# Performance work log

Hardware: AMD Instinct MI355X
Metric: run time of the kernel (lower is better)

The kernel has to match this reference:

```python
import jax, jax.numpy as jnp
import numpy as np

B, P, D_ENC, D_DEC, D_ATT, E, V, T = 64, 144, 1792, 512, 512, 300, 32000, 30
LN_EPS = 1e-5


def _ln(x, g, b):
    m = x.mean(-1, keepdims=True)
    v = jnp.var(x, axis=-1, keepdims=True)
    return (x - m) * jax.lax.rsqrt(v + LN_EPS) * g + b


def setup_inputs() -> dict:
    key = jax.random.key(0)
    ks = iter(jax.random.split(key, 40))
    r = lambda shape, s=0.02: (jax.random.normal(next(ks), shape, jnp.float32) * s)
    inp = {}
    inp['features'] = jax.random.normal(next(ks), (B, P, D_ENC), jnp.float32)
    inp['captions'] = jax.random.randint(next(ks), (B, T), 0, V, jnp.int32)
    inp['emb_table'] = r((V, E), 0.05)
    # attention params
    inp['ln_q_g'] = jnp.ones((D_DEC,), jnp.float32)
    inp['ln_q_b'] = jnp.zeros((D_DEC,), jnp.float32)
    inp['ln_kv_g'] = jnp.ones((D_ENC,), jnp.float32)
    inp['ln_kv_b'] = jnp.zeros((D_ENC,), jnp.float32)
    inp['Wq'] = r((D_DEC, D_ATT)); inp['bq'] = jnp.zeros((D_ATT,), jnp.float32)
    inp['Wk'] = r((D_ENC, D_ATT)); inp['bk'] = jnp.zeros((D_ATT,), jnp.float32)
    inp['Wbeta'] = r((D_DEC, 1)); inp['bbeta'] = jnp.zeros((1,), jnp.float32)
    # LSTM gate params, packed as [in_dim, 4*H] in gate order (i, f, o, g).
    # Context fed to the LSTM is the attention output of dim encoder_dim (V = normalized features).
    inp['Wh'] = r((D_DEC, 4 * D_DEC))
    inp['Wu'] = r((E, 4 * D_DEC))
    inp['Wa'] = r((D_ENC, 4 * D_DEC))
    inp['b_gates'] = jnp.zeros((4 * D_DEC,), jnp.float32)  # linear biases + extra b_* params combined
    # output head
    inp['W_Lh'] = r((D_DEC, E)); inp['b_Lh'] = jnp.zeros((E,), jnp.float32)
    inp['W_Lz'] = r((D_ENC, E)); inp['b_Lz'] = jnp.zeros((E,), jnp.float32)
    inp['W_Lo'] = r((E, V)); inp['b_Lo'] = jnp.zeros((V,), jnp.float32)
    # init state
    inp['W_ih'] = r((D_ENC, D_DEC)); inp['b_ih'] = jnp.zeros((D_DEC,), jnp.float32)
    inp['W_ic'] = r((D_ENC, D_DEC)); inp['b_ic'] = jnp.zeros((D_DEC,), jnp.float32)
    return inp


def reference(features, captions, emb_table, ln_q_g, ln_q_b, ln_kv_g, ln_kv_b,
              Wq, bq, Wk, bk, Wbeta, bbeta, Wh, Wu, Wa, b_gates,
              W_Lh, b_Lh, W_Lz, b_Lz, W_Lo, b_Lo, W_ih, b_ih, W_ic, b_ic):
    scale = jnp.sqrt(jnp.asarray(Wq.shape[1], jnp.float32))
    # features are constant across timesteps -> hoist ln_kv and K projection
    feats_n = _ln(features, ln_kv_g, ln_kv_b)          # [B,P,Denc]
    K = feats_n @ Wk + bk                               # [B,P,A]
    mean_a = features.mean(axis=1)                      # [B,Denc]
    h0 = mean_a @ W_ih + b_ih
    c0 = mean_a @ W_ic + b_ic
    embs = emb_table[captions]                          # [B,T,E] (dropout = identity in eval)
    xs = jnp.swapaxes(embs[:, :-1], 0, 1)               # [T-1,B,E], embedding at step t is word t-1

    def step(carry, emb_t):
        h, c = carry
        hq = _ln(h, ln_q_g, ln_q_b)                     # [B,H]
        Q = hq @ Wq + bq                                # [B,A]
        scores = jnp.einsum('ba,bpa->bp', Q, K) / scale
        alpha = jax.nn.softmax(scores, axis=-1)         # [B,P]
        context = jnp.einsum('bp,bpd->bd', alpha, feats_n)  # [B,Denc]
        beta = jax.nn.sigmoid(hq @ Wbeta + bbeta)       # [B,1]
        z = beta * context
        gates = h @ Wh + emb_t @ Wu + z @ Wa + b_gates  # [B,4H]
        i_t, f_t, o_t, g_t = jnp.split(gates, 4, axis=-1)
        c_new = jax.nn.sigmoid(f_t) * c + jax.nn.sigmoid(i_t) * jnp.tanh(g_t)
        h_new = jax.nn.sigmoid(o_t) * jnp.tanh(c_new)
        out_o = emb_t + (h_new @ W_Lh + b_Lh) + (z @ W_Lz + b_Lz)
        logits = out_o @ W_Lo + b_Lo                    # [B,V]
        return (h_new, c_new), (logits, alpha)

    _, (logits, alphas) = jax.lax.scan(step, (h0, c0), xs)
    # step t=0 stays zero, as in the original torch loop (range(1, seq_len))
    predictions = jnp.concatenate(
        [jnp.zeros((1,) + logits.shape[1:], logits.dtype), logits], axis=0).swapaxes(0, 1)
    alphas_out = jnp.concatenate(
        [jnp.zeros((1,) + alphas.shape[1:], alphas.dtype), alphas], axis=0).swapaxes(0, 1)
    return predictions, alphas_out
```

## Files before the change

### kernel.cpp

```cpp
#include <hip/hip_runtime.h>
#include <hip/hip_bf16.h>


#define NB 64
#define NP 144
#define DE 1792
#define DD 512
#define DA 512
#define EM 300
#define NV 32000
#define NTT 30
#define NS 29
#define G4 2048
#define KP 320
#define KG1 2304
#define LN_EPS 1e-5f
#define RSCALE 0.044194173824159216f
#define KSPL 12

typedef __attribute__((ext_vector_type(8))) short short8;
typedef __attribute__((ext_vector_type(4))) float f32x4;
typedef __attribute__((ext_vector_type(8))) unsigned short ushort8v;

__device__ __forceinline__ float bf2f(unsigned short u){
  union { unsigned int i; float f; } w; w.i = ((unsigned int)u) << 16; return w.f;
}
__device__ __forceinline__ unsigned short f2bf(float f){
  union { float f; unsigned int i; } u; u.f = f;
  unsigned int r = u.i + 0x7FFFu + ((u.i >> 16) & 1u);
  return (unsigned short)(r >> 16);
}
__device__ __forceinline__ float sigm(float x){ return 1.f/(1.f + __expf(-x)); }

__device__ __forceinline__ float wave_reduce_sum(float v){
  #pragma unroll
  for (int o = 32; o >= 1; o >>= 1) v += __shfl_xor(v, o);
  return v;
}
__device__ __forceinline__ float wave_reduce_max(float v){
  #pragma unroll
  for (int o = 32; o >= 1; o >>= 1) v = fmaxf(v, __shfl_xor(v, o));
  return v;
}
__device__ __forceinline__ float block_sum256(float v, float* sbuf){
  v = wave_reduce_sum(v);
  const int lane = threadIdx.x & 63, wid = threadIdx.x >> 6;
  if (lane == 0) sbuf[wid] = v;
  __syncthreads();
  const float r = sbuf[0] + sbuf[1] + sbuf[2] + sbuf[3];
  __syncthreads();
  return r;
}
__device__ __forceinline__ float block_sum512(float v, float* sbuf8){
  v = wave_reduce_sum(v);
  const int lane = threadIdx.x & 63, wid = threadIdx.x >> 6;
  if (lane == 0) sbuf8[wid] = v;
  __syncthreads();
  float r = 0.f;
  #pragma unroll
  for (int i = 0; i < 8; ++i) r += sbuf8[i];
  __syncthreads();
  return r;
}

__device__ __forceinline__ void stage_tile(const unsigned short* __restrict__ src,
    int row_stride, int k0, char* lds){
  const int tid = threadIdx.x;
  #pragma unroll
  for (int c = 0; c < 2; ++c){
    const int o = tid + c*256;
    const int m = o >> 3, ks8 = o & 7;
    const ushort8v v = *(const ushort8v*)&src[(size_t)m*row_stride + k0 + ks8*8];
    *(ushort8v*)&lds[m*128 + ((ks8 ^ (m&7))<<4)] = v;
  }
}
__device__ __forceinline__ void mma64(const char* Alds, const char* Blds,
    int w, int lane, f32x4 acc[4]){
  #pragma unroll
  for (int ks = 0; ks < 2; ++ks){
    const int slot = ks*4 + (lane>>4);
    const int n = w*16 + (lane&15);
    const short8 bfv = *(const short8*)&Blds[n*128 + ((slot ^ (n&7))<<4)];
    #pragma unroll
    for (int fm = 0; fm < 4; ++fm){
      const int m = fm*16 + (lane&15);
      const short8 afv = *(const short8*)&Alds[m*128 + ((slot ^ (m&7))<<4)];
      acc[fm] = __builtin_amdgcn_mfma_f32_16x16x32_bf16(afv, bfv, acc[fm], 0, 0, 0);
    }
  }
}

__global__ __launch_bounds__(256) void k_zero(float* __restrict__ pred,
                                              float* __restrict__ alph){
  const int idx = blockIdx.x * 256 + threadIdx.x;
  {
    const int b = idx / NV, v = idx - b * NV;
    pred[(size_t)b * NTT * NV + v] = 0.f;
  }
  if (idx < NB * NP){
    const int b = idx / NP, p = idx - b * NP;
    alph[(size_t)b * NTT * NP + p] = 0.f;
  }
}

__global__ __launch_bounds__(256) void k_ln_feats(const float* __restrict__ feats,
    const float* __restrict__ g, const float* __restrict__ bb,
    unsigned short* __restrict__ out){
  __shared__ float sbuf[4];
  const int row = blockIdx.x;
  const float* x = feats + (size_t)row * DE;
  float v[7]; float s = 0.f;
  #pragma unroll
  for (int i = 0; i < 7; ++i){ v[i] = x[i*256 + threadIdx.x]; s += v[i]; }
  const float mean = block_sum256(s, sbuf) * (1.f/DE);
  float q = 0.f;
  #pragma unroll
  for (int i = 0; i < 7; ++i){ const float d = v[i] - mean; q += d*d; }
  const float var = block_sum256(q, sbuf) * (1.f/DE);
  const float rinv = rsqrtf(var + LN_EPS);
  #pragma unroll
  for (int i = 0; i < 7; ++i){
    const int idx = i*256 + threadIdx.x;
    out[(size_t)row*DE + idx] = f2bf((v[i]-mean)*rinv*g[idx] + bb[idx]);
  }
}

__global__ __launch_bounds__(256) void k_mean(const float* __restrict__ feats,
                                              float* __restrict__ mean_a){
  const int idx = blockIdx.x * 256 + threadIdx.x;
  const int b = idx / DE, d = idx - b * DE;
  const float* p = feats + (size_t)b * NP * DE + d;
  float s = 0.f;
  for (int pp = 0; pp < NP; ++pp) s += p[(size_t)pp * DE];
  mean_a[idx] = s * (1.f/NP);
}

__global__ __launch_bounds__(256) void k_cvt_T(const float* __restrict__ src,
    unsigned short* __restrict__ dst, const int K, const int N, const int KPad){
  __shared__ float t[64][65];
  const int n0 = blockIdx.x*64, k0 = blockIdx.y*64;
  for (int i = threadIdx.x; i < 4096; i += 256){
    const int k = i>>6, n = i&63;
    t[k][n] = (k0 + k < K) ? src[(size_t)(k0+k)*N + n0+n] : 0.f;
  }
  __syncthreads();
  for (int i = threadIdx.x; i < 4096; i += 256){
    const int n = i>>6, k = i&63;
    dst[(size_t)(n0+n)*KPad + k0+k] = f2bf(t[k][n]);
  }
}

__global__ __launch_bounds__(256) void k_cvt_wlt(const float* __restrict__ W_Lh,
    const float* __restrict__ W_Lz, unsigned short* __restrict__ WLt){
  __shared__ float t[64][65];
  const int e0 = blockIdx.x*64, k0 = blockIdx.y*64;
  for (int i = threadIdx.x; i < 4096; i += 256){
    const int k = i>>6, e2 = i&63;
    const int kg = k0 + k, e = e0 + e2;
    float v = 0.f;
    if (e < EM) v = (kg < DD) ? W_Lh[(size_t)kg*EM + e] : W_Lz[(size_t)(kg-DD)*EM + e];
    t[k][e2] = v;
  }
  __syncthreads();
  for (int i = threadIdx.x; i < 4096; i += 256){
    const int e2 = i>>6, k = i&63;
    WLt[(size_t)(e0+e2)*KG1 + k0+k] = f2bf(t[k][e2]);
  }
}

__global__ __launch_bounds__(256) void k_wg(const float* __restrict__ Wq,
    const float* __restrict__ g, unsigned short* __restrict__ Wg){
  const int idx = blockIdx.x*256 + threadIdx.x;
  const int k = idx >> 9;
  Wg[idx] = f2bf(g[k]*Wq[idx]);
}

__global__ __launch_bounds__(512) void k_pre_vq(const float* __restrict__ Wq,
    const float* __restrict__ bk, float* __restrict__ vq){
  const int k = threadIdx.x;
  const float* row = Wq + (size_t)k*DA;
  float acc = 0.f;
  for (int a = 0; a < DA; ++a) acc = fmaf(row[a], bk[a], acc);
  vq[k] = acc;
}

__global__ __launch_bounds__(512) void k_uvoff(const float* __restrict__ Wq,
    const float* __restrict__ g, const float* __restrict__ bln,
    const float* __restrict__ bq, const float* __restrict__ Wbeta,
    const float* __restrict__ bbeta, const float* __restrict__ bk,
    float* __restrict__ u_, float* __restrict__ voff,
    float* __restrict__ gw, float* __restrict__ cscal){
  __shared__ float sbuf8[8];
  const int a = threadIdx.x;
  float uu = 0.f, vv = 0.f;
  for (int k = 0; k < DD; ++k){
    const float wv = Wq[(size_t)k*DA + a];
    uu = fmaf(g[k],   wv, uu);
    vv = fmaf(bln[k], wv, vv);
  }
  const float vo = vv + bq[a];
  u_[a]   = uu;
  voff[a] = vo;
  gw[a]   = g[a]*Wbeta[a];
  const float c1 = block_sum512(g[a]*Wbeta[a], sbuf8);
  const float c2 = block_sum512(bln[a]*Wbeta[a], sbuf8);
  const float c3 = block_sum512(uu*bk[a], sbuf8);
  const float c4 = block_sum512(vo*bk[a], sbuf8);
  if (a == 0){ cscal[0]=c1; cscal[1]=c2+bbeta[0]; cscal[2]=c3; cscal[3]=c4; }
}

__global__ __launch_bounds__(256) void k_KF(const unsigned short* __restrict__ fb,
    const unsigned short* __restrict__ WkT, unsigned short* __restrict__ KF){
  __shared__ char Alds[8192];
  __shared__ char Blds[8192];
  const int mt = blockIdx.x, nt = blockIdx.y;
  const int tid = threadIdx.x, w = tid>>6, lane = tid&63;
  f32x4 acc[4];
  #pragma unroll
  for (int i = 0; i < 4; ++i) acc[i] = (f32x4)(0.f);
  for (int kt = 0; kt < 28; ++kt){
    __syncthreads();
    stage_tile(fb  + (size_t)mt*64*DE, DE, kt*64, Alds);
    stage_tile(WkT + (size_t)nt*64*DE, DE, kt*64, Blds);
    __syncthreads();
    mma64(Alds, Blds, w, lane, acc);
  }
  const int q = nt*64 + w*16 + (lane&15);
  #pragma unroll
  for (int fm = 0; fm < 4; ++fm)
    #pragma unroll
    for (int r = 0; r < 4; ++r){
      const int row = mt*64 + fm*16 + (lane>>4)*4 + r;
      KF[(size_t)row*DD + q] = f2bf(acc[fm][r]);
    }
}

__global__ __launch_bounds__(256) void k_QG2(const unsigned short* __restrict__ KF,
    const unsigned short* __restrict__ Wg, const float* __restrict__ g_,
    const float* __restrict__ vq, unsigned short* __restrict__ G2){
  __shared__ char Alds[8192];
  __shared__ char Blds[8192];
  const int mt = blockIdx.x, nt = blockIdx.y;
  const int tid = threadIdx.x, w = tid>>6, lane = tid&63;
  f32x4 acc[4];
  #pragma unroll
  for (int i = 0; i < 4; ++i) acc[i] = (f32x4)(0.f);
  for (int kt = 0; kt < 8; ++kt){
    __syncthreads();
    stage_tile(KF + (size_t)mt*64*DD, DD, kt*64, Alds);
    stage_tile(Wg + (size_t)nt*64*DD, DD, kt*64, Blds);
    __syncthreads();
    mma64(Alds, Blds, w, lane, acc);
  }
  const int q = nt*64 + w*16 + (lane&15);
  const float add = g_[q]*vq[q];
  #pragma unroll
  for (int fm = 0; fm < 4; ++fm)
    #pragma unroll
    for (int r = 0; r < 4; ++r){
      const int row = mt*64 + fm*16 + (lane>>4)*4 + r;
      G2[(size_t)row*DD + q] = f2bf(acc[fm][r] + add);
    }
}

__global__ __launch_bounds__(512) void k_sc12(const unsigned short* __restrict__ KF,
    const float* __restrict__ u_, const float* __restrict__ voff,
    const float* __restrict__ cscal, float2* __restrict__ sc12){
  const int w = threadIdx.x>>6, lane = threadIdx.x&63;
  const int row = blockIdx.x*8 + w;
  const unsigned short* kf = KF + (size_t)row*DD + lane*8;
  float s1 = 0.f, s2 = 0.f;
  #pragma unroll
  for (int j = 0; j < 8; ++j){
    const float kv = bf2f(kf[j]);
    s1 = fmaf(u_[lane*8 + j],   kv, s1);
    s2 = fmaf(voff[lane*8 + j], kv, s2);
  }
  s1 = wave_reduce_sum(s1);
  s2 = wave_reduce_sum(s2);
  if (lane == 0){
    float2 o; o.x = s1 + cscal[2]; o.y = s2 + cscal[3];
    sc12[row] = o;
  }
}

__global__ __launch_bounds__(256) void k_init_g(const float* __restrict__ mean_a,
    const float* __restrict__ W, const float* __restrict__ bias,
    float* __restrict__ out, unsigned short* __restrict__ outbf){
  __shared__ float la[64*68];
  __shared__ float lb[64*68];
  const int j0 = blockIdx.x*64;
  const int tid = threadIdx.x, tr = tid&15, tn = tid>>4;
  float acc[16] = {0.f};
  for (int a0 = 0; a0 < DE; a0 += 64){
    __syncthreads();
    for (int i = tid; i < 4096; i += 256){
      const int b = i>>6, k = i&63;
      la[k*68 + b] = mean_a[(size_t)b*DE + a0+k];
    }
    for (int i = tid; i < 4096; i += 256){
      const int k = i>>6, j = i&63;
      lb[k*68 + j] = W[(size_t)(a0+k)*DD + j0+j];
    }
    __syncthreads();
    for (int k = 0; k < 64; ++k){
      float av[4], bv[4];
      #pragma unroll
      for (int ii = 0; ii < 4; ++ii) av[ii] = la[k*68 + tr*4+ii];
      #pragma unroll
      for (int jj = 0; jj < 4; ++jj) bv[jj] = lb[k*68 + tn*4+jj];
      #pragma unroll
      for (int ii = 0; ii < 4; ++ii)
        #pragma unroll
        for (int jj = 0; jj < 4; ++jj)
          acc[ii*4+jj] = fmaf(av[ii], bv[jj], acc[ii*4+jj]);
    }
  }
  #pragma unroll
  for (int ii = 0; ii < 4; ++ii)
    #pragma unroll
    for (int jj = 0; jj < 4; ++jj){
      const size_t idx = (size_t)(tr*4+ii)*DD + j0 + tn*4+jj;
      const float val = acc[ii*4+jj] + bias[j0 + tn*4+jj];
      out[idx] = val;
      if (outbf) outbf[idx] = f2bf(val);
    }
}

__global__ __launch_bounds__(256) void k_EU(const float* __restrict__ emb_table,
    const int* __restrict__ captions, const unsigned short* __restrict__ wut,
    float* __restrict__ eu){
  __shared__ char Alds[8192];
  __shared__ char Blds[8192];
  __shared__ int capL[64];
  const int jt = blockIdx.x, s = blockIdx.y;
  const int tid = threadIdx.x, w = tid>>6, lane = tid&63;
  if (tid < 64) capL[tid] = captions[tid*NTT + s];
  f32x4 acc[4];
  #pragma unroll
  for (int i = 0; i < 4; ++i) acc[i] = (f32x4)(0.f);
  for (int kt = 0; kt < 5; ++kt){
    __syncthreads();
    #pragma unroll
    for (int c = 0; c < 2; ++c){
      const int o = tid + c*256;
      const int m = o>>3, ks8 = o&7;
      const int e0 = kt*64 + ks8*8;
      const float* er = emb_table + (size_t)capL[m]*EM;
      ushort8v v;
      #pragma unroll
      for (int jj = 0; jj < 8; ++jj)
        v[jj] = (e0 + jj < EM) ? f2bf(er[e0 + jj]) : (unsigned short)0;
      *(ushort8v*)&Alds[m*128 + ((ks8 ^ (m&7))<<4)] = v;
    }
    stage_tile(wut + (size_t)jt*64*KP, KP, kt*64, Blds);
    __syncthreads();
    mma64(Alds, Blds, w, lane, acc);
  }
  const int j = jt*64 + w*16 + (lane&15);
  #pragma unroll
  for (int fm = 0; fm < 4; ++fm)
    #pragma unroll
    for (int r = 0; r < 4; ++r){
      const int b = fm*16 + (lane>>4)*4 + r;
      eu[((size_t)s*NB + b)*G4 + j] = acc[fm][r];
    }
}

__global__ __launch_bounds__(512) void k_A(
    const unsigned short* __restrict__ gp, const float* __restrict__ eu,
    const float* __restrict__ b_gates, const float* __restrict__ cin,
    float* __restrict__ cout, unsigned short* __restrict__ hst,
    const unsigned short* __restrict__ G2, const float2* __restrict__ sc12,
    const unsigned short* __restrict__ fb, const float* __restrict__ gw,
    const float* __restrict__ cscal, const int s, const int do_att,
    float* __restrict__ alph, unsigned short* __restrict__ zbf){
  __shared__ alignas(16) unsigned short hL[DD];
  __shared__ float sc[NP];
  __shared__ float al[NP];
  __shared__ float sredA[8*4];
  __shared__ float sbufM[8];
  __shared__ float sbufS[8];
  int sl, b;
  if (gridDim.x == 1){ sl = 0; b = blockIdx.y; }
  else {
    const int lin = blockIdx.x + 2*blockIdx.y;
    const int xcd = lin & 7, i = lin >> 3;
    b = xcd*8 + (i & 7);
    sl = i >> 3;
  }
  const int tid = threadIdx.x;
  const int w = tid>>6, lane = tid&63;
  float hn;
  if (s == 0){
    const unsigned short hb = hst[(size_t)b*DD + tid];
    hn = bf2f(hb);
    hL[tid] = hb;
  } else {
    const int m = s - 1;
    unsigned short gv[4*KSPL];
    #pragma unroll
    for (int ks = 0; ks < KSPL; ++ks){
      const unsigned short* gr = gp + ((size_t)ks*NB + b)*G4 + tid;
      gv[ks*4+0] = gr[0];
      gv[ks*4+1] = gr[DD];
      gv[ks*4+2] = gr[2*DD];
      gv[ks*4+3] = gr[3*DD];
    }
    const float* eur = eu + ((size_t)m*NB + b)*G4 + tid;
    float gs0 = b_gates[tid]        + eur[0];
    float gs1 = b_gates[DD + tid]   + eur[DD];
    float gs2 = b_gates[2*DD + tid] + eur[2*DD];
    float gs3 = b_gates[3*DD + tid] + eur[3*DD];
    #pragma unroll
    for (int ks = 0; ks < KSPL; ++ks){
      gs0 += bf2f(gv[ks*4+0]); gs1 += bf2f(gv[ks*4+1]);
      gs2 += bf2f(gv[ks*4+2]); gs3 += bf2f(gv[ks*4+3]);
    }
    const size_t idx = (size_t)b*DD + tid;
    const float cn = sigm(gs1)*cin[idx] + sigm(gs0)*tanhf(gs3);
    hn = sigm(gs2)*tanhf(cn);
    cout[idx] = cn;
    const unsigned short hb = f2bf(hn);
    hst[(size_t)s*NB*DD + idx] = hb;
    hL[tid] = hb;
  }
  if (!do_att) return;
  float p1 = hn, p2 = hn*hn, p3 = hn*gw[tid];
  #pragma unroll
  for (int o = 32; o >= 1; o >>= 1){
    p1 += __shfl_xor(p1, o);
    p2 += __shfl_xor(p2, o);
    p3 += __shfl_xor(p3, o);
  }
  if (lane == 0){ sredA[w*4] = p1; sredA[w*4+1] = p2; sredA[w*4+2] = p3; }
  __syncthreads();
  float S1 = 0.f, S2 = 0.f, S3 = 0.f;
  #pragma unroll
  for (int i = 0; i < 8; ++i){
    S1 += sredA[i*4]; S2 += sredA[i*4+1]; S3 += sredA[i*4+2];
  }
  const float mean = S1*(1.f/512.f);
  const float var  = S2*(1.f/512.f) - mean*mean;
  const float rinv = rsqrtf(var + LN_EPS);
  const float beta = sigm(rinv*(S3 - mean*cscal[0]) + cscal[1]);
  const short8 hv = *(const short8*)&hL[lane*8];
  #pragma unroll 1
  for (int i0 = 0; i0 < 18; i0 += 6){
    short8 U[6];
    float2 SV[6];
    #pragma unroll
    for (int j = 0; j < 6; ++j){
      const int p = w + 8*(i0+j);
      U[j] = *(const short8*)&G2[(size_t)(b*NP + p)*DD + lane*8];
      if (lane == 0) SV[j] = sc12[b*NP + p];
    }
    #pragma unroll
    for (int j = 0; j < 6; ++j){
      float a2 = 0.f;
      #pragma unroll
      for (int q = 0; q < 8; ++q)
        a2 = fmaf(bf2f((unsigned short)U[j][q]), bf2f((unsigned short)hv[q]), a2);
      a2 = wave_reduce_sum(a2);
      if (lane == 0)
        sc[w + 8*(i0+j)] = RSCALE*(rinv*a2 - rinv*mean*SV[j].x + SV[j].y);
    }
  }
  __syncthreads();
  const float v = (tid < NP) ? sc[tid] : -1e30f;
  const float mv = wave_reduce_max(v);
  if (lane == 0) sbufM[w] = mv;
  __syncthreads();
  float mm = sbufM[0];
  #pragma unroll
  for (int i = 1; i < 8; ++i) mm = fmaxf(mm, sbufM[i]);
  const float e = (tid < NP) ? __expf(v - mm) : 0.f;
  const float sv = wave_reduce_sum(e);
  if (lane == 0) sbufS[w] = sv;
  __syncthreads();
  float ssum = 0.f;
  #pragma unroll
  for (int i = 0; i < 8; ++i) ssum += sbufS[i];
  if (tid < NP){
    const float a3 = e / ssum;
    al[tid] = a3;
    if (sl == 0) alph[((size_t)b*NTT + s + 1)*NP + tid] = a3;
  }
  __syncthreads();
  if (tid < 448){
    const int d0 = sl*896 + tid*2;
    const unsigned short* fB = fb + (size_t)b*NP*DE + d0;
    float a0 = 0.f, a1 = 0.f;
    #pragma unroll 1
    for (int p0 = 0; p0 < NP; p0 += 12){
      ushort2 fv[12];
      #pragma unroll
      for (int j = 0; j < 12; ++j) fv[j] = *(const ushort2*)&fB[(size_t)(p0+j)*DE];
      #pragma unroll
      for (int j = 0; j < 12; ++j){
        const float ap = al[p0+j];
        a0 = fmaf(ap, bf2f(fv[j].x), a0);
        a1 = fmaf(ap, bf2f(fv[j].y), a1);
      }
    }
    ushort2 zo;
    zo.x = f2bf(a0*beta);
    zo.y = f2bf(a1*beta);
    *(ushort2*)&zbf[((size_t)s*NB + b)*DE + d0] = zo;
  }
}

__global__ __launch_bounds__(256) void k_B(
    const unsigned short* __restrict__ hst, const unsigned short* __restrict__ zbf,
    const unsigned short* __restrict__ whT, const unsigned short* __restrict__ wat,
    const int s, unsigned short* __restrict__ gp){
  __shared__ char Alds[8192];
  __shared__ char Blds[8192];
  const int jt = blockIdx.x, ks = blockIdx.y;
  const int tid = threadIdx.x, w = tid>>6, lane = tid&63;
  const unsigned short* hrow = hst + (size_t)s*NB*DD;
  const unsigned short* zrow = zbf + (size_t)s*NB*DE;
  f32x4 acc[4];
  #pragma unroll
  for (int i = 0; i < 4; ++i) acc[i] = (f32x4)(0.f);
  for (int kt = 0; kt < 3; ++kt){
    const int k0 = ks*192 + kt*64;
    __syncthreads();
    if (k0 < DD) stage_tile(hrow, DD, k0, Alds);
    else         stage_tile(zrow, DE, k0 - DD, Alds);
    #pragma unroll
    for (int c2 = 0; c2 < 2; ++c2){
      const int o = tid + c2*256;
      const int m = o>>3, ks8 = o&7;
      const int col = (m>>4)*DD + jt*16 + (m&15);
      const unsigned short* src = (k0 < DD)
          ? whT + (size_t)col*DD + k0
          : wat + (size_t)col*DE + (k0 - DD);
      const ushort8v v = *(const ushort8v*)&src[ks8*8];
      *(ushort8v*)&Blds[m*128 + ((ks8 ^ (m&7))<<4)] = v;
    }
    __syncthreads();
    mma64(Alds, Blds, w, lane, acc);
  }
  const int jcol = jt*16 + (lane&15);
  unsigned short* gps = gp + (size_t)ks*NB*G4;
  #pragma unroll
  for (int fm = 0; fm < 4; ++fm)
    #pragma unroll
    for (int r = 0; r < 4; ++r){
      const int b = fm*16 + (lane>>4)*4 + r;
      gps[(size_t)b*G4 + w*DD + jcol] = f2bf(acc[fm][r]);
    }
}

__global__ __launch_bounds__(256) void k_G1m(const unsigned short* __restrict__ hstbf,
    const unsigned short* __restrict__ zbf, const unsigned short* __restrict__ WLt,
    float* __restrict__ g1p){
  __shared__ char Alds[8192];
  __shared__ char Blds[8192];
  const int e0 = blockIdx.x*64, s = blockIdx.y, ks6 = blockIdx.z;
  const int tid = threadIdx.x, w = tid>>6, lane = tid&63;
  const unsigned short* hrow = hstbf + (size_t)(s+1)*NB*DD;
  const unsigned short* zrow = zbf + (size_t)s*NB*DE;
  f32x4 acc[4];
  #pragma unroll
  for (int i = 0; i < 4; ++i) acc[i] = (f32x4)(0.f);
  for (int kt = 0; kt < 6; ++kt){
    const int k0 = ks6*384 + kt*64;
    __syncthreads();
    if (k0 < DD) stage_tile(hrow, DD, k0, Alds);
    else         stage_tile(zrow, DE, k0 - DD, Alds);
    stage_tile(WLt + (size_t)e0*KG1, KG1, k0, Blds);
    __syncthreads();
    mma64(Alds, Blds, w, lane, acc);
  }
  const int e = e0 + w*16 + (lane&15);
  float* dst = g1p + (size_t)ks6*NS*NB*KP;
  #pragma unroll
  for (int fm = 0; fm < 4; ++fm)
    #pragma unroll
    for (int r = 0; r < 4; ++r){
      const int b = fm*16 + (lane>>4)*4 + r;
      dst[((size_t)s*NB + b)*KP + e] = acc[fm][r];
    }
}

__global__ __launch_bounds__(256) void k_G1red(const float* __restrict__ g1p,
    const float* __restrict__ b_Lh, const float* __restrict__ b_Lz,
    const float* __restrict__ emb_table, const int* __restrict__ captions,
    unsigned short* __restrict__ outo){
  const int idx = blockIdx.x*256 + threadIdx.x;
  const int row = idx / KP, e = idx - row*KP;
  const int s = row >> 6, b = row & 63;
  float v = 0.f;
  #pragma unroll
  for (int ks6 = 0; ks6 < 6; ++ks6) v += g1p[(size_t)ks6*NS*NB*KP + idx];
  if (e < EM){
    const int cap = captions[b*NTT + s];
    v += b_Lh[e] + b_Lz[e] + emb_table[(size_t)cap*EM + e];
  } else v = 0.f;
  outo[idx] = f2bf(v);
}

__global__ __launch_bounds__(256) void k_G2(const unsigned short* __restrict__ Abf,
    const unsigned short* __restrict__ Bt, const float* __restrict__ b_Lo,
    float* __restrict__ pred){
  __shared__ char Alds[128*128];
  __shared__ char Blds[256*128];
  const int bid = blockIdx.x;
  const int xcd = bid & 7, idx8 = bid >> 3;
  const int wgid = (xcd < 3 ? xcd*235 : 705 + (xcd-3)*234) + idx8;
  const int nt = wgid / 15, mt = wgid - nt*15;
  const int tid = threadIdx.x, w = tid>>6, lane = tid&63;
  f32x4 acc[8][4];
  #pragma unroll
  for (int i = 0; i < 8; ++i)
    #pragma unroll
    for (int j = 0; j < 4; ++j)
      acc[i][j] = (f32x4)(0.f);
  for (int kt = 0; kt < 5; ++kt){
    const int k0 = kt*64;
    __syncthreads();
    #pragma unroll
    for (int c2 = 0; c2 < 4; ++c2){
      const int o16 = tid + c2*256;
      const int m = o16>>3, ks8 = o16&7;
      const ushort8v v = *(const ushort8v*)&Abf[(size_t)(mt*128+m)*KP + k0 + ks8*8];
      *(ushort8v*)&Alds[m*128 + ((ks8 ^ (m&7))<<4)] = v;
    }
    #pragma unroll
    for (int c2 = 0; c2 < 8; ++c2){
      const int o16 = tid + c2*256;
      const int n = o16>>3, ks8 = o16&7;
      const ushort8v v = *(const ushort8v*)&Bt[(size_t)(nt*256+n)*KP + k0 + ks8*8];
      *(ushort8v*)&Blds[n*128 + ((ks8 ^ (n&7))<<4)] = v;
    }
    __syncthreads();
    #pragma unroll
    for (int ks = 0; ks < 2; ++ks){
      const int slot = ks*4 + (lane>>4);
      short8 af[8];
      #pragma unroll
      for (int fm = 0; fm < 8; ++fm){
        const int m = fm*16 + (lane&15);
        af[fm] = *(const short8*)&Alds[m*128 + ((slot ^ (m&7))<<4)];
      }
      #pragma unroll
      for (int fn = 0; fn < 4; ++fn){
        const int n = w*64 + fn*16 + (lane&15);
        const short8 bfv = *(const short8*)&Blds[n*128 + ((slot ^ (n&7))<<4)];
        #pragma unroll
        for (int fm = 0; fm < 8; ++fm)
          acc[fm][fn] = __builtin_amdgcn_mfma_f32_16x16x32_bf16(af[fm], bfv, acc[fm][fn], 0, 0, 0);
      }
    }
  }
  const int ncol0 = nt*256 + w*64 + (lane&15);
  #pragma unroll
  for (int fm = 0; fm < 8; ++fm){
    #pragma unroll
    for (int r = 0; r < 4; ++r){
      const int row = mt*128 + fm*16 + (lane>>4)*4 + r;
      if (row < NS*NB){
        const int s = row >> 6, b = row & 63;
        float* prow = &pred[((size_t)b*NTT + s + 1)*NV + ncol0];
        #pragma unroll
        for (int fn = 0; fn < 4; ++fn)
          __builtin_nontemporal_store(acc[fm][fn][r] + b_Lo[ncol0 + fn*16],
                                      &prow[fn*16]);
      }
    }
  }
}

extern "C" void kernel_launch(void* const* d_in, const int* in_sizes, int n_in,
                              void* d_out, int out_size, void* d_ws, size_t ws_size,
                              hipStream_t stream){
  const float* features  = (const float*)d_in[0];
  const int*   captions  = (const int*)  d_in[1];
  const float* emb_table = (const float*)d_in[2];
  const float* ln_q_g = (const float*)d_in[3];
  const float* ln_q_b = (const float*)d_in[4];
  const float* ln_kv_g= (const float*)d_in[5];
  const float* ln_kv_b= (const float*)d_in[6];
  const float* Wq     = (const float*)d_in[7];
  const float* bq     = (const float*)d_in[8];
  const float* Wk     = (const float*)d_in[9];
  const float* bk     = (const float*)d_in[10];
  const float* Wbeta  = (const float*)d_in[11];
  const float* bbeta  = (const float*)d_in[12];
  const float* Wh     = (const float*)d_in[13];
  const float* Wu     = (const float*)d_in[14];
  const float* Wa     = (const float*)d_in[15];
  const float* b_gates= (const float*)d_in[16];
  const float* W_Lh   = (const float*)d_in[17];
  const float* b_Lh   = (const float*)d_in[18];
  const float* W_Lz   = (const float*)d_in[19];
  const float* b_Lz   = (const float*)d_in[20];
  const float* W_Lo   = (const float*)d_in[21];
  const float* b_Lo   = (const float*)d_in[22];
  const float* W_ih   = (const float*)d_in[23];
  const float* b_ih   = (const float*)d_in[24];
  const float* W_ic   = (const float*)d_in[25];
  const float* b_ic   = (const float*)d_in[26];

  float* pred = (float*)d_out;
  float* alph = pred + (size_t)NB * NTT * NV;

  char* w = (char*)d_ws;
  auto alloc = [&](size_t bytes) -> void* {
    void* p = (void*)w; w += (bytes + 255) & ~(size_t)255; return p;
  };
  unsigned short* feats_bf = (unsigned short*)alloc((size_t)NB*NP*DE * 2);
  unsigned short* wlo_t    = (unsigned short*)alloc((size_t)NV*KP * 2);
  unsigned short* whT      = (unsigned short*)alloc((size_t)G4*DD * 2);
  unsigned short* wut      = (unsigned short*)alloc((size_t)G4*KP * 2);
  unsigned short* wat      = (unsigned short*)alloc((size_t)G4*DE * 2);
  unsigned short* WkT      = (unsigned short*)alloc((size_t)DD*DE * 2);
  unsigned short* WLt      = (unsigned short*)alloc((size_t)KP*KG1 * 2);
  unsigned short* Wg       = (unsigned short*)alloc((size_t)DD*DD * 2);
  unsigned short* KFbf     = (unsigned short*)alloc((size_t)NB*NP*DD * 2);
  unsigned short* G2bf     = (unsigned short*)alloc((size_t)NB*NP*DD * 2);
  float2* sc12  = (float2*)alloc((size_t)NB*NP * 8);
  float* vq     = (float*)alloc((size_t)DD * 4);
  float* u_     = (float*)alloc((size_t)DD * 4);
  float* voff   = (float*)alloc((size_t)DD * 4);
  float* gw     = (float*)alloc((size_t)DD * 4);
  float* cscal  = (float*)alloc(16);
  float* mean_a = (float*)alloc((size_t)NB*DE * 4);
  float* hbuf   = (float*)alloc((size_t)NB*DD * 4);
  float* cb0    = (float*)alloc((size_t)NB*DD * 4);
  float* cb1    = (float*)alloc((size_t)NB*DD * 4);
  unsigned short* hstbf = (unsigned short*)alloc((size_t)(NS+1)*NB*DD * 2);
  unsigned short* zbf   = (unsigned short*)alloc((size_t)NS*NB*DE * 2);
  unsigned short* outo  = (unsigned short*)alloc((size_t)1920*KP * 2);
  unsigned short* gp    = (unsigned short*)alloc((size_t)KSPL*NB*G4 * 2);
  float* eu_all = (float*)alloc((size_t)NS*NB*G4 * 4);
  float* g1p    = (float*)alloc((size_t)6*NS*NB*KP * 4);
  float* cb[2] = { cb0, cb1 };

  k_zero<<<dim3((NB*NV)/256), dim3(256), 0, stream>>>(pred, alph);
  k_ln_feats<<<dim3(NB*NP), dim3(256), 0, stream>>>(features, ln_kv_g, ln_kv_b, feats_bf);
  k_mean<<<dim3((NB*DE)/256), dim3(256), 0, stream>>>(features, mean_a);
  k_cvt_T<<<dim3(NV/64, KP/64), dim3(256), 0, stream>>>(W_Lo, wlo_t, EM, NV, KP);
  k_cvt_T<<<dim3(G4/64, DD/64), dim3(256), 0, stream>>>(Wh, whT, DD, G4, DD);
  k_cvt_T<<<dim3(G4/64, KP/64), dim3(256), 0, stream>>>(Wu, wut, EM, G4, KP);
  k_cvt_T<<<dim3(G4/64, DE/64), dim3(256), 0, stream>>>(Wa, wat, DE, G4, DE);
  k_cvt_T<<<dim3(DD/64, DE/64), dim3(256), 0, stream>>>(Wk, WkT, DE, DD, DE);
  k_cvt_wlt<<<dim3(KP/64, KG1/64), dim3(256), 0, stream>>>(W_Lh, W_Lz, WLt);
  k_wg<<<dim3((DD*DD)/256), dim3(256), 0, stream>>>(Wq, ln_q_g, Wg);
  k_pre_vq<<<dim3(1), dim3(512), 0, stream>>>(Wq, bk, vq);
  k_uvoff<<<dim3(1), dim3(512), 0, stream>>>(Wq, ln_q_g, ln_q_b, bq, Wbeta, bbeta,
      bk, u_, voff, gw, cscal);
  k_KF<<<dim3(NB*NP/64, DD/64), dim3(256), 0, stream>>>(feats_bf, WkT, KFbf);
  k_QG2<<<dim3(NB*NP/64, DD/64), dim3(256), 0, stream>>>(KFbf, Wg, ln_q_g, vq, G2bf);
  k_sc12<<<dim3(NB*NP/8), dim3(512), 0, stream>>>(KFbf, u_, voff, cscal, sc12);
  k_init_g<<<dim3(DD/64), dim3(256), 0, stream>>>(mean_a, W_ih, b_ih, hbuf, hstbf);
  k_init_g<<<dim3(DD/64), dim3(256), 0, stream>>>(mean_a, W_ic, b_ic, cb0, nullptr);
  k_EU<<<dim3(G4/64, NS), dim3(256), 0, stream>>>(emb_table, captions, wut, eu_all);

  for (int s = 0; s < NS; ++s){
    k_A<<<dim3(2, NB), dim3(512), 0, stream>>>(gp, eu_all, b_gates,
        cb[(s & 1) ^ 1], cb[s & 1], hstbf, G2bf, sc12, feats_bf,
        gw, cscal, s, 1, alph, zbf);
    k_B<<<dim3(32, KSPL), dim3(256), 0, stream>>>(hstbf, zbf, whT, wat, s, gp);
  }
  k_A<<<dim3(1, NB), dim3(512), 0, stream>>>(gp, eu_all, b_gates,
      cb[(NS & 1) ^ 1], cb[NS & 1], hstbf, G2bf, sc12, feats_bf,
      gw, cscal, NS, 0, alph, zbf);

  k_G1m<<<dim3(5, NS, 6), dim3(256), 0, stream>>>(hstbf, zbf, WLt, g1p);
  k_G1red<<<dim3((NS*NB*KP)/256), dim3(256), 0, stream>>>(g1p, b_Lh, b_Lz,
      emb_table, captions, outo);
  k_G2<<<dim3(1875), dim3(256), 0, stream>>>(outo, wlo_t, b_Lo, pred);
}
```

Before: 1.318 ms.

## Use 128x256 MFMA tiles with XCD-aware block mapping for K/G2 GEMMs

The K-projection and G2 GEMMs move from 64x64 tiles on a 144x8 grid to 128x256 tiles on 144 blocks, reusing the shared gemm_big routine (factored out of the logits GEMM). Block ids are remapped so consecutive blocks spread across the eight XCDs. The larger tiles cut redundant global loads and raise MFMA work per LDS stage, but leave only 144 blocks on the device. Separately, the per-step attention kernel batches more loads in flight (9 G2 rows and 36 feature rows per iteration), which raises register pressure.

```diff
diff --git a/kernel.cpp b/kernel.cpp
--- a/kernel.cpp
+++ b/kernel.cpp
@@ -90,6 +90,50 @@
   }
 }
 
+template <int NKT>
+__device__ __forceinline__ void gemm_big(const unsigned short* __restrict__ A,
+    const unsigned short* __restrict__ B, int sa, int sb,
+    char* Alds, char* Blds, int mt, int nt, f32x4 acc[8][4]){
+  const int tid = threadIdx.x, w = tid>>6, lane = tid&63;
+  for (int kt = 0; kt < NKT; ++kt){
+    const int k0 = kt*64;
+    __syncthreads();
+    #pragma unroll
+    for (int c2 = 0; c2 < 4; ++c2){
+      const int o16 = tid + c2*256;
+      const int m = o16>>3, ks8 = o16&7;
+      const ushort8v v = *(const ushort8v*)&A[(size_t)(mt*128+m)*sa + k0 + ks8*8];
+      *(ushort8v*)&Alds[m*128 + ((ks8 ^ (m&7))<<4)] = v;
+    }
+    #pragma unroll
+    for (int c2 = 0; c2 < 8; ++c2){
+      const int o16 = tid + c2*256;
+      const int n = o16>>3, ks8 = o16&7;
+      const ushort8v v = *(const ushort8v*)&B[(size_t)(nt*256+n)*sb + k0 + ks8*8];
+      *(ushort8v*)&Blds[n*128 + ((ks8 ^ (n&7))<<4)] = v;
+    }
+    __syncthreads();
+    #pragma unroll
+    for (int ks = 0; ks < 2; ++ks){
+      const int slot = ks*4 + (lane>>4);
+      short8 af[8];
+      #pragma unroll
+      for (int fm = 0; fm < 8; ++fm){
+        const int m = fm*16 + (lane&15);
+        af[fm] = *(const short8*)&Alds[m*128 + ((slot ^ (m&7))<<4)];
+      }
+      #pragma unroll
+      for (int fn = 0; fn < 4; ++fn){
+        const int n = w*64 + fn*16 + (lane&15);
+        const short8 bfv = *(const short8*)&Blds[n*128 + ((slot ^ (n&7))<<4)];
+        #pragma unroll
+        for (int fm = 0; fm < 8; ++fm)
+          acc[fm][fn] = __builtin_amdgcn_mfma_f32_16x16x32_bf16(af[fm], bfv, acc[fm][fn], 0, 0, 0);
+      }
+    }
+  }
+}
+
 __global__ __launch_bounds__(256) void k_zero(float* __restrict__ pred,
                                               float* __restrict__ alph){
   const int idx = blockIdx.x * 256 + threadIdx.x;
@@ -211,55 +255,60 @@
 
 __global__ __launch_bounds__(256) void k_KF(const unsigned short* __restrict__ fb,
     const unsigned short* __restrict__ WkT, unsigned short* __restrict__ KF){
-  __shared__ char Alds[8192];
-  __shared__ char Blds[8192];
-  const int mt = blockIdx.x, nt = blockIdx.y;
+  __shared__ char Alds[128*128];
+  __shared__ char Blds[256*128];
+  const int bid = blockIdx.x;
+  const int wgid = (bid & 7)*18 + (bid >> 3);
+  const int nt = wgid & 1, mt = wgid >> 1;
   const int tid = threadIdx.x, w = tid>>6, lane = tid&63;
-  f32x4 acc[4];
-  #pragma unroll
-  for (int i = 0; i < 4; ++i) acc[i] = (f32x4)(0.f);
-  for (int kt = 0; kt < 28; ++kt){
-    __syncthreads();
-    stage_tile(fb  + (size_t)mt*64*DE, DE, kt*64, Alds);
-    stage_tile(WkT + (size_t)nt*64*DE, DE, kt*64, Blds);
-    __syncthreads();
-    mma64(Alds, Blds, w, lane, acc);
-  }
-  const int q = nt*64 + w*16 + (lane&15);
-  #pragma unroll
-  for (int fm = 0; fm < 4; ++fm)
+  f32x4 acc[8][4];
+  #pragma unroll
+  for (int i = 0; i < 8; ++i)
+    #pragma unroll
+    for (int j = 0; j < 4; ++j) acc[i][j] = (f32x4)(0.f);
+  gemm_big<28>(fb, WkT, DE, DE, Alds, Blds, mt, nt, acc);
+  const int ncol0 = nt*256 + w*64 + (lane&15);
+  #pragma unroll
+  for (int fm = 0; fm < 8; ++fm)
     #pragma unroll
     for (int r = 0; r < 4; ++r){
-      const int row = mt*64 + fm*16 + (lane>>4)*4 + r;
-      KF[(size_t)row*DD + q] = f2bf(acc[fm][r]);
+      const int row = mt*128 + fm*16 + (lane>>4)*4 + r;
+      #pragma unroll
+      for (int fn = 0; fn < 4; ++fn)
+        KF[(size_t)row*DD + ncol0 + fn*16] = f2bf(acc[fm][fn][r]);
     }
 }
 
 __global__ __launch_bounds__(256) void k_QG2(const unsigned short* __restrict__ KF,
     const unsigned short* __restrict__ Wg, const float* __restrict__ g_,
     const float* __restrict__ vq, unsigned short* __restrict__ G2){
-  __shared__ char Alds[8192];
-  __shared__ char Blds[8192];
-  const int mt = blockIdx.x, nt = blockIdx.y;
+  __shared__ char Alds[128*128];
+  __shared__ char Blds[256*128];
+  const int bid = blockIdx.x;
+  const int wgid = (bid & 7)*18 + (bid >> 3);
+  const int nt = wgid & 1, mt = wgid >> 1;
   const int tid = threadIdx.x, w = tid>>6, lane = tid&63;
-  f32x4 acc[4];
-  #pragma unroll
-  for (int i = 0; i < 4; ++i) acc[i] = (f32x4)(0.f);
-  for (int kt = 0; kt < 8; ++kt){
-    __syncthreads();
-    stage_tile(KF + (size_t)mt*64*DD, DD, kt*64, Alds);
-    stage_tile(Wg + (size_t)nt*64*DD, DD, kt*64, Blds);
-    __syncthreads();
-    mma64(Alds, Blds, w, lane, acc);
-  }
-  const int q = nt*64 + w*16 + (lane&15);
-  const float add = g_[q]*vq[q];
-  #pragma unroll
-  for (int fm = 0; fm < 4; ++fm)
+  f32x4 acc[8][4];
+  #pragma unroll
+  for (int i = 0; i < 8; ++i)
+    #pragma unroll
+    for (int j = 0; j < 4; ++j) acc[i][j] = (f32x4)(0.f);
+  gemm_big<8>(KF, Wg, DD, DD, Alds, Blds, mt, nt, acc);
+  const int ncol0 = nt*256 + w*64 + (lane&15);
+  float addv[4];
+  #pragma unroll
+  for (int fn = 0; fn < 4; ++fn){
+    const int q = ncol0 + fn*16;
+    addv[fn] = g_[q]*vq[q];
+  }
+  #pragma unroll
+  for (int fm = 0; fm < 8; ++fm)
     #pragma unroll
     for (int r = 0; r < 4; ++r){
-      const int row = mt*64 + fm*16 + (lane>>4)*4 + r;
-      G2[(size_t)row*DD + q] = f2bf(acc[fm][r] + add);
+      const int row = mt*128 + fm*16 + (lane>>4)*4 + r;
+      #pragma unroll
+      for (int fn = 0; fn < 4; ++fn)
+        G2[(size_t)row*DD + ncol0 + fn*16] = f2bf(acc[fm][fn][r] + addv[fn]);
     }
 }
 
@@ -446,17 +495,17 @@
   const float beta = sigm(rinv*(S3 - mean*cscal[0]) + cscal[1]);
   const short8 hv = *(const short8*)&hL[lane*8];
   #pragma unroll 1
-  for (int i0 = 0; i0 < 18; i0 += 6){
-    short8 U[6];
-    float2 SV[6];
-    #pragma unroll
-    for (int j = 0; j < 6; ++j){
+  for (int i0 = 0; i0 < 18; i0 += 9){
+    short8 U[9];
+    float2 SV[9];
+    #pragma unroll
+    for (int j = 0; j < 9; ++j){
       const int p = w + 8*(i0+j);
       U[j] = *(const short8*)&G2[(size_t)(b*NP + p)*DD + lane*8];
       if (lane == 0) SV[j] = sc12[b*NP + p];
     }
     #pragma unroll
-    for (int j = 0; j < 6; ++j){
+    for (int j = 0; j < 9; ++j){
       float a2 = 0.f;
       #pragma unroll
       for (int q = 0; q < 8; ++q)
@@ -492,12 +541,12 @@
     const unsigned short* fB = fb + (size_t)b*NP*DE + d0;
     float a0 = 0.f, a1 = 0.f;
     #pragma unroll 1
-    for (int p0 = 0; p0 < NP; p0 += 12){
-      ushort2 fv[12];
-      #pragma unroll
-      for (int j = 0; j < 12; ++j) fv[j] = *(const ushort2*)&fB[(size_t)(p0+j)*DE];
-      #pragma unroll
-      for (int j = 0; j < 12; ++j){
+    for (int p0 = 0; p0 < NP; p0 += 36){
+      ushort2 fv[36];
+      #pragma unroll
+      for (int j = 0; j < 36; ++j) fv[j] = *(const ushort2*)&fB[(size_t)(p0+j)*DE];
+      #pragma unroll
+      for (int j = 0; j < 36; ++j){
         const float ap = al[p0+j];
         a0 = fmaf(ap, bf2f(fv[j].x), a0);
         a1 = fmaf(ap, bf2f(fv[j].y), a1);
@@ -618,43 +667,7 @@
     #pragma unroll
     for (int j = 0; j < 4; ++j)
       acc[i][j] = (f32x4)(0.f);
-  for (int kt = 0; kt < 5; ++kt){
-    const int k0 = kt*64;
-    __syncthreads();
-    #pragma unroll
-    for (int c2 = 0; c2 < 4; ++c2){
-      const int o16 = tid + c2*256;
-      const int m = o16>>3, ks8 = o16&7;
-      const ushort8v v = *(const ushort8v*)&Abf[(size_t)(mt*128+m)*KP + k0 + ks8*8];
-      *(ushort8v*)&Alds[m*128 + ((ks8 ^ (m&7))<<4)] = v;
-    }
-    #pragma unroll
-    for (int c2 = 0; c2 < 8; ++c2){
-      const int o16 = tid + c2*256;
-      const int n = o16>>3, ks8 = o16&7;
-      const ushort8v v = *(const ushort8v*)&Bt[(size_t)(nt*256+n)*KP + k0 + ks8*8];
-      *(ushort8v*)&Blds[n*128 + ((ks8 ^ (n&7))<<4)] = v;
-    }
-    __syncthreads();
-    #pragma unroll
-    for (int ks = 0; ks < 2; ++ks){
-      const int slot = ks*4 + (lane>>4);
-      short8 af[8];
-      #pragma unroll
-      for (int fm = 0; fm < 8; ++fm){
-        const int m = fm*16 + (lane&15);
-        af[fm] = *(const short8*)&Alds[m*128 + ((slot ^ (m&7))<<4)];
-      }
-      #pragma unroll
-      for (int fn = 0; fn < 4; ++fn){
-        const int n = w*64 + fn*16 + (lane&15);
-        const short8 bfv = *(const short8*)&Blds[n*128 + ((slot ^ (n&7))<<4)];
-        #pragma unroll
-        for (int fm = 0; fm < 8; ++fm)
-          acc[fm][fn] = __builtin_amdgcn_mfma_f32_16x16x32_bf16(af[fm], bfv, acc[fm][fn], 0, 0, 0);
-      }
-    }
-  }
+  gemm_big<5>(Abf, Bt, KP, KP, Alds, Blds, mt, nt, acc);
   const int ncol0 = nt*256 + w*64 + (lane&15);
   #pragma unroll
   for (int fm = 0; fm < 8; ++fm){
@@ -752,8 +765,8 @@
   k_pre_vq<<<dim3(1), dim3(512), 0, stream>>>(Wq, bk, vq);
   k_uvoff<<<dim3(1), dim3(512), 0, stream>>>(Wq, ln_q_g, ln_q_b, bq, Wbeta, bbeta,
       bk, u_, voff, gw, cscal);
-  k_KF<<<dim3(NB*NP/64, DD/64), dim3(256), 0, stream>>>(feats_bf, WkT, KFbf);
-  k_QG2<<<dim3(NB*NP/64, DD/64), dim3(256), 0, stream>>>(KFbf, Wg, ln_q_g, vq, G2bf);
+  k_KF<<<dim3(144), dim3(256), 0, stream>>>(feats_bf, WkT, KFbf);
+  k_QG2<<<dim3(144), dim3(256), 0, stream>>>(KFbf, Wg, ln_q_g, vq, G2bf);
   k_sc12<<<dim3(NB*NP/8), dim3(512), 0, stream>>>(KFbf, u_, voff, cscal, sc12);
   k_init_g<<<dim3(DD/64), dim3(256), 0, stream>>>(mean_a, W_ih, b_ih, hbuf, hstbf);
   k_init_g<<<dim3(DD/64), dim3(256), 0, stream>>>(mean_a, W_ic, b_ic, cb0, nullptr);
```

Result: faster. 1.284 ms (-2.6%).
